# Kernel optimization log

Hardware: AMD Instinct MI355X
Metric: run time of the kernel (lower is better)

The kernel has to match this reference:

```python
import jax, jax.numpy as jnp
import numpy as np
import math


def setup_inputs() -> dict:
    key = jax.random.key(0)
    k0, k1, k2, k3, k4 = jax.random.split(key, 5)
    in_f, out_f, nb = 512, 512, 8
    B, S = 4, 2048
    x = jax.random.normal(k0, (B, S, in_f), dtype=jnp.float32)
    # RBF params (frozen in original: basis_trainable=False)
    fan_in = in_f  # fan_in of rbf.weight.T which is (num_basis, in_features)
    bound = 1.0 / math.sqrt(fan_in)
    rbf_weight = jax.random.uniform(k1, (in_f, nb), dtype=jnp.float32,
                                    minval=-math.sqrt(3.0) * 0.33 / math.sqrt(fan_in),
                                    maxval=math.sqrt(3.0) * 0.33 / math.sqrt(fan_in))
    rbf_centers = jnp.tile(jnp.linspace(-bound, bound, nb, dtype=jnp.float32)[None, :], (in_f, 1))
    # KAN spline weight (in, nb, out); fan_in for init is in_f*nb
    fan2 = in_f * nb
    wb = math.sqrt(3.0) * 0.33 / math.sqrt(fan2)
    weight = jax.random.uniform(k2, (in_f, nb, out_f), dtype=jnp.float32, minval=-wb, maxval=wb)
    bias = jax.random.uniform(k3, (out_f,), dtype=jnp.float32,
                              minval=-1.0 / math.sqrt(fan2), maxval=1.0 / math.sqrt(fan2))
    scale_base = jax.random.uniform(k4, (in_f, out_f), dtype=jnp.float32, minval=-0.1, maxval=0.1)
    return {"x": x, "rbf_weight": rbf_weight, "rbf_centers": rbf_centers,
            "weight": weight, "bias": bias, "scale_base": scale_base}


def reference(x, rbf_weight, rbf_centers, weight, bias, scale_base):
    in_f = x.shape[-1]
    nb = rbf_weight.shape[1]
    beta = (nb / math.log2(nb)) ** 2  # get_rbf_width(2/nb, log2(nb))
    batch_shape = x.shape[:-1]
    xf = x.reshape(-1, in_f)  # (N, in)
    # RBF basis expansion: (N, in, nb)
    z = xf[:, :, None] * rbf_weight[None, :, :] - rbf_centers[None, :, :]
    phi = jnp.exp(-beta * (z * z))
    # spline contraction + base path, expressed as efficient contractions
    y = jnp.einsum('nib,ibo->no', phi, weight)
    y = y + bias + jnp.cos(xf) @ scale_base
    return y.reshape(*batch_shape, weight.shape[-1])
```

## Files before the change

### kernel.cpp

```cpp
#include <hip/hip_runtime.h>
#include <hip/hip_bf16.h>

typedef __attribute__((ext_vector_type(8))) short short8;
typedef __attribute__((ext_vector_type(4))) float f32x4;

#define IN_F 512
#define OUT_F 512
#define BM 64
#define BN 512
#define BK 64
#define THREADS 512
#define PHI_STEPS 64
#define NSTEPS 72
#define KSPLIT 2
#define SPL (NSTEPS / KSPLIT)
#define IMG_CHUNKS 4096
#define A_SH (BM * BK)
#define B_SH (BN * BK)
#define PART_ELEMS (8192 * OUT_F)

__device__ __forceinline__ short f2bf(float f) {
  __hip_bfloat16 h = __float2bfloat16(f);
  return __builtin_bit_cast(short, h);
}

__device__ __forceinline__ void glds16(const void* g, void* l) {
  __builtin_amdgcn_global_load_lds(
      (const __attribute__((address_space(1))) unsigned int*)g,
      (__attribute__((address_space(3))) unsigned int*)l, 16, 0, 0);
}

__device__ __forceinline__ float bsrc(const float* __restrict__ w,
                                      const float* __restrict__ sb,
                                      int k, int col) {
  return (k < IN_F * 8) ? w[(size_t)k * OUT_F + col]
                        : sb[(size_t)(k - IN_F * 8) * OUT_F + col];
}

__global__ void __launch_bounds__(256) prep_b(const float* __restrict__ w,
                                              const float* __restrict__ sb,
                                              short* __restrict__ img) {
  const int D = blockIdx.x * 256 + threadIdx.x;
  const int ci = D & (IMG_CHUNKS - 1);
  const int s = D >> 12;
  const int n = ci >> 3, slot = ci & 7;
  const int oct = slot ^ (n & 7);
  short8 v;
#pragma unroll
  for (int j = 0; j < 8; ++j) v[j] = f2bf(bsrc(w, sb, s * 64 + oct * 8 + j, n));
  *(short8*)&img[(size_t)D * 8] = v;
}

__global__ void __launch_bounds__(256) reduce_add(const float* __restrict__ part,
                                                  float* __restrict__ out) {
  const int n4 = PART_ELEMS / 4;
  const float4* p4 = (const float4*)part;
  float4* o4 = (float4*)out;
  for (int i = blockIdx.x * 256 + threadIdx.x; i < n4; i += gridDim.x * 256) {
    float4 a = o4[i];
    const float4 b = p4[i];
    a.x += b.x; a.y += b.y; a.z += b.z; a.w += b.w;
    o4[i] = a;
  }
}

template <int KS, bool PREB>
__global__ void __launch_bounds__(THREADS, 2) kan_main(
    const float* __restrict__ x, const float* __restrict__ rw,
    const float* __restrict__ rc, const float* __restrict__ w,
    const float* __restrict__ bias, const float* __restrict__ sb,
    const short* __restrict__ bimg, float* __restrict__ out,
    float* __restrict__ part) {
  __shared__ __align__(16) short A_lds[2][A_SH];
  __shared__ __align__(16) short B_lds[2][B_SH];

  const int t = threadIdx.x, lane = t & 63, wid = t >> 6;
  const int l15 = lane & 15, kb = lane >> 4;
  const int m0 = blockIdx.x * BM;
  const int ks = (KS == 2) ? blockIdx.y : 0;
  const int s0 = ks * SPL;

  const int a_il = t & 7;
  const int a_m = t >> 3;
  const float c2 = -10.2591705f;

  f32x4 acc[4][4];
#pragma unroll
  for (int i = 0; i < 4; ++i)
#pragma unroll
    for (int j = 0; j < 4; ++j) acc[i][j] = (f32x4){0.f, 0.f, 0.f, 0.f};

  auto stage = [&](int s, short* __restrict__ Ad, short* __restrict__ Bd) {
    if (PREB) {
      const short* src = bimg + ((size_t)s * IMG_CHUNKS + t) * 8;
#pragma unroll
      for (int c = 0; c < 8; ++c)
        glds16(src + (size_t)c * 512 * 8, Bd + c * 4096 + wid * 512);
    } else {
#pragma unroll
      for (int c = 0; c < 8; ++c) {
        const int ci = c * 512 + t;
        const int n = ci >> 3, slot = ci & 7, oct = slot ^ (n & 7);
        short8 v;
#pragma unroll
        for (int j = 0; j < 8; ++j) v[j] = f2bf(bsrc(w, sb, s * 64 + oct * 8 + j, n));
        *(short8*)&Bd[ci * 8] = v;
      }
    }
    short8 av;
    if (s < PHI_STEPS) {
      const int feat = s * 8 + a_il;
      const float xv = x[(size_t)(m0 + a_m) * IN_F + feat];
      const float4 r0 = *(const float4*)(rw + feat * 8);
      const float4 r1 = *(const float4*)(rw + feat * 8 + 4);
      const float4 q0 = *(const float4*)(rc + feat * 8);
      const float4 q1 = *(const float4*)(rc + feat * 8 + 4);
      const float rwv[8] = {r0.x, r0.y, r0.z, r0.w, r1.x, r1.y, r1.z, r1.w};
      const float rcv[8] = {q0.x, q0.y, q0.z, q0.w, q1.x, q1.y, q1.z, q1.w};
#pragma unroll
      for (int b = 0; b < 8; ++b) {
        const float z = fmaf(xv, rwv[b], -rcv[b]);
        av[b] = f2bf(exp2f(c2 * z * z));
      }
    } else {
      const float* xp = x + (size_t)(m0 + a_m) * IN_F + (s - PHI_STEPS) * 64 + a_il * 8;
      const float4 xa = *(const float4*)xp;
      const float4 xb = *(const float4*)(xp + 4);
      av[0] = f2bf(__cosf(xa.x)); av[1] = f2bf(__cosf(xa.y));
      av[2] = f2bf(__cosf(xa.z)); av[3] = f2bf(__cosf(xa.w));
      av[4] = f2bf(__cosf(xb.x)); av[5] = f2bf(__cosf(xb.y));
      av[6] = f2bf(__cosf(xb.z)); av[7] = f2bf(__cosf(xb.w));
    }
    Ad[a_m * BK + (a_il ^ (a_m & 7)) * 8 + 0] = av[0];
    *(short8*)&Ad[a_m * BK + (a_il ^ (a_m & 7)) * 8] = av;
  };

  auto mfma_step = [&](const short* __restrict__ Ab, const short* __restrict__ Bb) {
#pragma unroll
    for (int kk = 0; kk < 2; ++kk) {
      const int sk = kk * 4 + kb;
      short8 af[4], bf[4];
#pragma unroll
      for (int mi = 0; mi < 4; ++mi) {
        const int r = mi * 16 + l15;
        af[mi] = *(const short8*)&Ab[r * BK + (sk ^ (r & 7)) * 8];
      }
#pragma unroll
      for (int ni = 0; ni < 4; ++ni) {
        const int n = wid * 64 + ni * 16 + l15;
        bf[ni] = *(const short8*)&Bb[n * BK + (sk ^ (n & 7)) * 8];
      }
#pragma unroll
      for (int mi = 0; mi < 4; ++mi)
#pragma unroll
        for (int ni = 0; ni < 4; ++ni)
          acc[mi][ni] = __builtin_amdgcn_mfma_f32_16x16x32_bf16(
              af[mi], bf[ni], acc[mi][ni], 0, 0, 0);
    }
  };

  stage(s0, A_lds[0], B_lds[0]);
  __syncthreads();
#pragma unroll 2
  for (int si = 0; si < SPL; ++si) {
    const int cur = si & 1;
    if (si + 1 < SPL) stage(s0 + si + 1, A_lds[cur ^ 1], B_lds[cur ^ 1]);
    mfma_step(A_lds[cur], B_lds[cur]);
    __syncthreads();
  }

#pragma unroll
  for (int ni = 0; ni < 4; ++ni) {
    const int col = wid * 64 + ni * 16 + l15;
    const float bb = (KS == 1 || ks == 0) ? bias[col] : 0.f;
#pragma unroll
    for (int mi = 0; mi < 4; ++mi) {
      const int rb = m0 + mi * 16 + kb * 4;
#pragma unroll
      for (int r4 = 0; r4 < 4; ++r4) {
        const size_t idx = (size_t)(rb + r4) * OUT_F + col;
        if (KS == 1 || ks == 0) out[idx] = acc[mi][ni][r4] + bb;
        else                    part[idx] = acc[mi][ni][r4];
      }
    }
  }
}

extern "C" void kernel_launch(void* const* d_in, const int* in_sizes, int n_in,
                              void* d_out, int out_size, void* d_ws, size_t ws_size,
                              hipStream_t stream) {
  const float* x    = (const float*)d_in[0];
  const float* rw   = (const float*)d_in[1];
  const float* rc   = (const float*)d_in[2];
  const float* w    = (const float*)d_in[3];
  const float* bias = (const float*)d_in[4];
  const float* sb   = (const float*)d_in[5];
  float* out = (float*)d_out;

  const int nrows = in_sizes[0] / IN_F;

  const size_t img_bytes  = (size_t)NSTEPS * IMG_CHUNKS * 16;
  const size_t part_bytes = (size_t)PART_ELEMS * sizeof(float);
  const int img_chunks_total = NSTEPS * IMG_CHUNKS;

  if (ws_size >= img_bytes + part_bytes) {
    short* img = (short*)d_ws;
    float* part = (float*)((char*)d_ws + img_bytes);
    prep_b<<<img_chunks_total / 256, 256, 0, stream>>>(w, sb, img);
    dim3 grid(nrows / BM, KSPLIT);
    kan_main<KSPLIT, true><<<grid, THREADS, 0, stream>>>(x, rw, rc, w, bias, sb,
                                                         img, out, part);
    reduce_add<<<2048, 256, 0, stream>>>(part, out);
  } else if (ws_size >= part_bytes) {
    float* part = (float*)d_ws;
    dim3 grid(nrows / BM, KSPLIT);
    kan_main<KSPLIT, false><<<grid, THREADS, 0, stream>>>(x, rw, rc, w, bias, sb,
                                                          nullptr, out, part);
    reduce_add<<<2048, 256, 0, stream>>>(part, out);
  } else {
    dim3 grid(nrows / BM, 1);
    kan_main<1, false><<<grid, THREADS, 0, stream>>>(x, rw, rc, w, bias, sb,
                                                     nullptr, out, nullptr);
  }
}
```

Measured before the change: 85.15 us.

## Rewrite KAN kernel with 256x256 tiles, 4-way K-split, bf16 partials

Replaces the 64-row, full-N tile kernel with 1024-thread blocks computing 256x256 output tiles over a 4-way K-split. A new pre-pass transposes x into a per-feature layout so it can be streamed into LDS with async global-to-LDS loads, and each wave computes phi for one feature octet across rows. Partial sums from three of the splits are stored as bf16 and combined by a three-way reduce kernel. Barriers and waitcnts are placed by hand. The aim is more reuse of A and B per tile and less partial-sum traffic. The costs are an extra transpose pass, a larger workspace, lost precision in the bf16 partials, and the removal of the workspace-size fallbacks.

```diff
diff --git a/kernel.cpp b/kernel.cpp
--- a/kernel.cpp
+++ b/kernel.cpp
@@ -6,28 +6,32 @@
 
 #define IN_F 512
 #define OUT_F 512
-#define BM 64
-#define BN 512
-#define BK 64
-#define THREADS 512
 #define PHI_STEPS 64
 #define NSTEPS 72
-#define KSPLIT 2
-#define SPL (NSTEPS / KSPLIT)
-#define IMG_CHUNKS 4096
-#define A_SH (BM * BK)
-#define B_SH (BN * BK)
+#define BCH2 2048
+#define NT2 2
+#define KT 18
 #define PART_ELEMS (8192 * OUT_F)
+#define C2 (-10.2591705f)
 
 __device__ __forceinline__ short f2bf(float f) {
-  __hip_bfloat16 h = __float2bfloat16(f);
-  return __builtin_bit_cast(short, h);
+  unsigned u = __builtin_bit_cast(unsigned, f);
+  u += 0x7fffu + ((u >> 16) & 1u);
+  return (short)(u >> 16);
+}
+__device__ __forceinline__ float b2f(unsigned short u) {
+  return __builtin_bit_cast(float, (unsigned)u << 16);
 }
 
 __device__ __forceinline__ void glds16(const void* g, void* l) {
   __builtin_amdgcn_global_load_lds(
       (const __attribute__((address_space(1))) unsigned int*)g,
       (__attribute__((address_space(3))) unsigned int*)l, 16, 0, 0);
+}
+__device__ __forceinline__ void glds4(const void* g, void* l) {
+  __builtin_amdgcn_global_load_lds(
+      (const __attribute__((address_space(1))) unsigned int*)g,
+      (__attribute__((address_space(3))) unsigned int*)l, 4, 0, 0);
 }
 
 __device__ __forceinline__ float bsrc(const float* __restrict__ w,
@@ -37,52 +41,86 @@
                         : sb[(size_t)(k - IN_F * 8) * OUT_F + col];
 }
 
-__global__ void __launch_bounds__(256) prep_b(const float* __restrict__ w,
-                                              const float* __restrict__ sb,
-                                              short* __restrict__ img) {
+__global__ void __launch_bounds__(256) prep_b2(const float* __restrict__ w,
+                                               const float* __restrict__ sb,
+                                               short* __restrict__ img) {
   const int D = blockIdx.x * 256 + threadIdx.x;
-  const int ci = D & (IMG_CHUNKS - 1);
-  const int s = D >> 12;
+  const int ci = D & (BCH2 - 1);
+  const int im = D >> 11;
+  const int s = im % NSTEPS;
+  const int nt = im / NSTEPS;
   const int n = ci >> 3, slot = ci & 7;
   const int oct = slot ^ (n & 7);
+  const int col = nt * 256 + n;
   short8 v;
 #pragma unroll
-  for (int j = 0; j < 8; ++j) v[j] = f2bf(bsrc(w, sb, s * 64 + oct * 8 + j, n));
+  for (int j = 0; j < 8; ++j) v[j] = f2bf(bsrc(w, sb, s * 64 + oct * 8 + j, col));
   *(short8*)&img[(size_t)D * 8] = v;
 }
 
-__global__ void __launch_bounds__(256) reduce_add(const float* __restrict__ part,
-                                                  float* __restrict__ out) {
+__global__ void __launch_bounds__(256) prep_x(const float* __restrict__ x,
+                                              float* __restrict__ ximg) {
+  __shared__ float T[256][17];
+  const int t = threadIdx.x;
+  const int s2 = blockIdx.x;
+  const int blk = blockIdx.y;
+#pragma unroll
+  for (int rep = 0; rep < 4; ++rep) {
+    const int row = rep * 64 + (t >> 2);
+    const int p = t & 3;
+    const float4 v = *(const float4*)&x[(size_t)(blk * 256 + row) * IN_F + s2 * 16 + p * 4];
+    T[row][p * 4 + 0] = v.x; T[row][p * 4 + 1] = v.y;
+    T[row][p * 4 + 2] = v.z; T[row][p * 4 + 3] = v.w;
+  }
+  __syncthreads();
+#pragma unroll
+  for (int f = 0; f < 16; ++f) {
+    const int s = 2 * s2 + (f >> 3), oct = f & 7;
+    ximg[(size_t)s * 65536 + oct * 8192 + blk * 256 + t] = T[t][f];
+  }
+}
+
+__global__ void __launch_bounds__(256) reduce3b(const short* __restrict__ part,
+                                                float* __restrict__ out) {
+  typedef __attribute__((ext_vector_type(4))) short short4v;
   const int n4 = PART_ELEMS / 4;
-  const float4* p4 = (const float4*)part;
+  const short4v* p0 = (const short4v*)part;
+  const short4v* p1 = (const short4v*)(part + PART_ELEMS);
+  const short4v* p2 = (const short4v*)(part + 2 * (size_t)PART_ELEMS);
   float4* o4 = (float4*)out;
   for (int i = blockIdx.x * 256 + threadIdx.x; i < n4; i += gridDim.x * 256) {
     float4 a = o4[i];
-    const float4 b = p4[i];
-    a.x += b.x; a.y += b.y; a.z += b.z; a.w += b.w;
+    const short4v q0 = p0[i], q1 = p1[i], q2 = p2[i];
+    a.x += b2f((unsigned short)q0[0]) + b2f((unsigned short)q1[0]) + b2f((unsigned short)q2[0]);
+    a.y += b2f((unsigned short)q0[1]) + b2f((unsigned short)q1[1]) + b2f((unsigned short)q2[1]);
+    a.z += b2f((unsigned short)q0[2]) + b2f((unsigned short)q1[2]) + b2f((unsigned short)q2[2]);
+    a.w += b2f((unsigned short)q0[3]) + b2f((unsigned short)q1[3]) + b2f((unsigned short)q2[3]);
     o4[i] = a;
   }
 }
 
-template <int KS, bool PREB>
-__global__ void __launch_bounds__(THREADS, 2) kan_main(
-    const float* __restrict__ x, const float* __restrict__ rw,
-    const float* __restrict__ rc, const float* __restrict__ w,
-    const float* __restrict__ bias, const float* __restrict__ sb,
-    const short* __restrict__ bimg, float* __restrict__ out,
-    float* __restrict__ part) {
-  __shared__ __align__(16) short A_lds[2][A_SH];
-  __shared__ __align__(16) short B_lds[2][B_SH];
+__device__ __forceinline__ f32x4 MFMA(short8 a, short8 b, f32x4 c) {
+  return __builtin_amdgcn_mfma_f32_16x16x32_bf16(a, b, c, 0, 0, 0);
+}
+
+__global__ void __launch_bounds__(1024, 4) kan_fx(
+    const float* __restrict__ x, const float* __restrict__ ximg,
+    const float* __restrict__ rw, const float* __restrict__ rc,
+    const short* __restrict__ bimg, const float* __restrict__ bias,
+    float* __restrict__ out, short* __restrict__ part) {
+  __shared__ __align__(16) short A_lds[2][256 * 64];
+  __shared__ __align__(16) short B_lds[2][256 * 64];
+  __shared__ __align__(16) float X_lds[2][2048];
 
   const int t = threadIdx.x, lane = t & 63, wid = t >> 6;
+  const int wm = wid >> 2, wn = wid & 3;
   const int l15 = lane & 15, kb = lane >> 4;
-  const int m0 = blockIdx.x * BM;
-  const int ks = (KS == 2) ? blockIdx.y : 0;
-  const int s0 = ks * SPL;
-
-  const int a_il = t & 7;
-  const int a_m = t >> 3;
-  const float c2 = -10.2591705f;
+  const int mb = blockIdx.x, nt = blockIdx.y, ks = blockIdx.z;
+  const int m0 = mb * 256, n0 = nt * 256, s0 = ks * KT;
+
+  const int octu = __builtin_amdgcn_readfirstlane(wid >> 1);
+  const int h = wid & 1;
+  const int r1 = h * 128 + lane, r2 = r1 + 64;
 
   f32x4 acc[4][4];
 #pragma unroll
@@ -90,97 +128,130 @@
 #pragma unroll
     for (int j = 0; j < 4; ++j) acc[i][j] = (f32x4){0.f, 0.f, 0.f, 0.f};
 
-  auto stage = [&](int s, short* __restrict__ Ad, short* __restrict__ Bd) {
-    if (PREB) {
-      const short* src = bimg + ((size_t)s * IMG_CHUNKS + t) * 8;
-#pragma unroll
-      for (int c = 0; c < 8; ++c)
-        glds16(src + (size_t)c * 512 * 8, Bd + c * 4096 + wid * 512);
-    } else {
-#pragma unroll
-      for (int c = 0; c < 8; ++c) {
-        const int ci = c * 512 + t;
-        const int n = ci >> 3, slot = ci & 7, oct = slot ^ (n & 7);
-        short8 v;
-#pragma unroll
-        for (int j = 0; j < 8; ++j) v[j] = f2bf(bsrc(w, sb, s * 64 + oct * 8 + j, n));
-        *(short8*)&Bd[ci * 8] = v;
-      }
-    }
-    short8 av;
-    if (s < PHI_STEPS) {
-      const int feat = s * 8 + a_il;
-      const float xv = x[(size_t)(m0 + a_m) * IN_F + feat];
-      const float4 r0 = *(const float4*)(rw + feat * 8);
-      const float4 r1 = *(const float4*)(rw + feat * 8 + 4);
-      const float4 q0 = *(const float4*)(rc + feat * 8);
-      const float4 q1 = *(const float4*)(rc + feat * 8 + 4);
-      const float rwv[8] = {r0.x, r0.y, r0.z, r0.w, r1.x, r1.y, r1.z, r1.w};
-      const float rcv[8] = {q0.x, q0.y, q0.z, q0.w, q1.x, q1.y, q1.z, q1.w};
-#pragma unroll
-      for (int b = 0; b < 8; ++b) {
-        const float z = fmaf(xv, rwv[b], -rcv[b]);
-        av[b] = f2bf(exp2f(c2 * z * z));
-      }
-    } else {
-      const float* xp = x + (size_t)(m0 + a_m) * IN_F + (s - PHI_STEPS) * 64 + a_il * 8;
-      const float4 xa = *(const float4*)xp;
-      const float4 xb = *(const float4*)(xp + 4);
-      av[0] = f2bf(__cosf(xa.x)); av[1] = f2bf(__cosf(xa.y));
-      av[2] = f2bf(__cosf(xa.z)); av[3] = f2bf(__cosf(xa.w));
-      av[4] = f2bf(__cosf(xb.x)); av[5] = f2bf(__cosf(xb.y));
-      av[6] = f2bf(__cosf(xb.z)); av[7] = f2bf(__cosf(xb.w));
-    }
-    Ad[a_m * BK + (a_il ^ (a_m & 7)) * 8 + 0] = av[0];
-    *(short8*)&Ad[a_m * BK + (a_il ^ (a_m & 7)) * 8] = av;
-  };
-
-  auto mfma_step = [&](const short* __restrict__ Ab, const short* __restrict__ Bb) {
+  float rwv[8], rcv[8];
+
+  auto loadP = [&](int s1) {
+    const int feat = s1 * 8 + octu;
+#pragma unroll
+    for (int j = 0; j < 8; ++j) { rwv[j] = rw[feat * 8 + j]; rcv[j] = rc[feat * 8 + j]; }
+  };
+  auto stageX = [&](int s1, int buf) {
+    const float* base = ximg + (size_t)s1 * 65536 + octu * 8192 + mb * 256 + h * 128;
+    glds4(base + lane, &X_lds[buf][wid * 128]);
+    glds4(base + 64 + lane, &X_lds[buf][wid * 128 + 64]);
+  };
+  auto stageB = [&](int s1, int buf) {
+#pragma unroll
+    for (int c = 0; c < 2; ++c) {
+      const short* src = bimg + (((size_t)nt * NSTEPS + s1) * BCH2 + c * 1024 + t) * 8;
+      glds16(src, &B_lds[buf][c * 8192 + wid * 512]);
+    }
+  };
+  auto writeA_phi = [&](int buf) {
+    const float xa = X_lds[buf][wid * 128 + lane];
+    const float xb = X_lds[buf][wid * 128 + 64 + lane];
+    short8 va, vb;
+#pragma unroll
+    for (int b = 0; b < 8; ++b) {
+      const float za = fmaf(xa, rwv[b], -rcv[b]);
+      const float zb = fmaf(xb, rwv[b], -rcv[b]);
+      va[b] = f2bf(exp2f(C2 * za * za));
+      vb[b] = f2bf(exp2f(C2 * zb * zb));
+    }
+    *(short8*)&A_lds[buf][r1 * 64 + (octu ^ (r1 & 7)) * 8] = va;
+    *(short8*)&A_lds[buf][r2 * 64 + (octu ^ (r2 & 7)) * 8] = vb;
+  };
+  auto writeA_cos = [&](int buf, const float4& a0, const float4& a1,
+                        const float4& b0, const float4& b1) {
+    short8 va, vb;
+    va[0] = f2bf(__cosf(a0.x)); va[1] = f2bf(__cosf(a0.y));
+    va[2] = f2bf(__cosf(a0.z)); va[3] = f2bf(__cosf(a0.w));
+    va[4] = f2bf(__cosf(a1.x)); va[5] = f2bf(__cosf(a1.y));
+    va[6] = f2bf(__cosf(a1.z)); va[7] = f2bf(__cosf(a1.w));
+    vb[0] = f2bf(__cosf(b0.x)); vb[1] = f2bf(__cosf(b0.y));
+    vb[2] = f2bf(__cosf(b0.z)); vb[3] = f2bf(__cosf(b0.w));
+    vb[4] = f2bf(__cosf(b1.x)); vb[5] = f2bf(__cosf(b1.y));
+    vb[6] = f2bf(__cosf(b1.z)); vb[7] = f2bf(__cosf(b1.w));
+    *(short8*)&A_lds[buf][r1 * 64 + (octu ^ (r1 & 7)) * 8] = va;
+    *(short8*)&A_lds[buf][r2 * 64 + (octu ^ (r2 & 7)) * 8] = vb;
+  };
+  auto mma = [&](int buf) {
 #pragma unroll
     for (int kk = 0; kk < 2; ++kk) {
       const int sk = kk * 4 + kb;
       short8 af[4], bf[4];
 #pragma unroll
       for (int mi = 0; mi < 4; ++mi) {
-        const int r = mi * 16 + l15;
-        af[mi] = *(const short8*)&Ab[r * BK + (sk ^ (r & 7)) * 8];
+        const int r = wm * 64 + mi * 16 + l15;
+        af[mi] = *(const short8*)&A_lds[buf][r * 64 + (sk ^ (r & 7)) * 8];
       }
 #pragma unroll
       for (int ni = 0; ni < 4; ++ni) {
-        const int n = wid * 64 + ni * 16 + l15;
-        bf[ni] = *(const short8*)&Bb[n * BK + (sk ^ (n & 7)) * 8];
+        const int n = wn * 64 + ni * 16 + l15;
+        bf[ni] = *(const short8*)&B_lds[buf][n * 64 + (sk ^ (n & 7)) * 8];
       }
 #pragma unroll
       for (int mi = 0; mi < 4; ++mi)
 #pragma unroll
         for (int ni = 0; ni < 4; ++ni)
-          acc[mi][ni] = __builtin_amdgcn_mfma_f32_16x16x32_bf16(
-              af[mi], bf[ni], acc[mi][ni], 0, 0, 0);
-    }
-  };
-
-  stage(s0, A_lds[0], B_lds[0]);
-  __syncthreads();
-#pragma unroll 2
-  for (int si = 0; si < SPL; ++si) {
-    const int cur = si & 1;
-    if (si + 1 < SPL) stage(s0 + si + 1, A_lds[cur ^ 1], B_lds[cur ^ 1]);
-    mfma_step(A_lds[cur], B_lds[cur]);
-    __syncthreads();
+          acc[mi][ni] = MFMA(af[mi], bf[ni], acc[mi][ni]);
+    }
+  };
+
+  loadP(s0);
+  stageX(s0, 0);
+  stageB(s0, 0);
+  asm volatile("s_waitcnt vmcnt(2)" ::: "memory");
+  writeA_phi(0);
+  asm volatile("s_waitcnt lgkmcnt(0)" ::: "memory");
+
+  for (int si = 0; si < KT; ++si) {
+    const int b = si & 1;
+    const int s = s0 + si;
+    const bool hasN = (si + 1 < KT);
+    const bool nPhi = (s + 1 < PHI_STEPS);
+    float4 ca0, ca1, cb0, cb1;
+    if (hasN) {
+      if (nPhi) {
+        loadP(s + 1);
+        stageX(s + 1, b ^ 1);
+        stageB(s + 1, b ^ 1);
+        asm volatile("s_waitcnt vmcnt(4)" ::: "memory");
+      } else {
+        const int f0 = (s + 1 - PHI_STEPS) * 64 + octu * 8;
+        const float* xr1 = x + (size_t)(m0 + r1) * IN_F + f0;
+        const float* xr2 = x + (size_t)(m0 + r2) * IN_F + f0;
+        ca0 = *(const float4*)xr1; ca1 = *(const float4*)(xr1 + 4);
+        cb0 = *(const float4*)xr2; cb1 = *(const float4*)(xr2 + 4);
+        stageB(s + 1, b ^ 1);
+        asm volatile("s_waitcnt vmcnt(2)" ::: "memory");
+      }
+    } else {
+      asm volatile("s_waitcnt vmcnt(0)" ::: "memory");
+    }
+    __builtin_amdgcn_s_barrier();
+    mma(b);
+    if (hasN) {
+      asm volatile("s_waitcnt vmcnt(2)" ::: "memory");
+      if (nPhi) writeA_phi(b ^ 1);
+      else      writeA_cos(b ^ 1, ca0, ca1, cb0, cb1);
+      asm volatile("s_waitcnt lgkmcnt(0)" ::: "memory");
+    }
+    __builtin_amdgcn_s_barrier();
   }
 
 #pragma unroll
   for (int ni = 0; ni < 4; ++ni) {
-    const int col = wid * 64 + ni * 16 + l15;
-    const float bb = (KS == 1 || ks == 0) ? bias[col] : 0.f;
+    const int col = n0 + wn * 64 + ni * 16 + l15;
+    const float bb = (ks == 0) ? bias[col] : 0.f;
 #pragma unroll
     for (int mi = 0; mi < 4; ++mi) {
-      const int rb = m0 + mi * 16 + kb * 4;
+      const int rb = m0 + wm * 64 + mi * 16 + kb * 4;
 #pragma unroll
       for (int r4 = 0; r4 < 4; ++r4) {
         const size_t idx = (size_t)(rb + r4) * OUT_F + col;
-        if (KS == 1 || ks == 0) out[idx] = acc[mi][ni][r4] + bb;
-        else                    part[idx] = acc[mi][ni][r4];
+        if (ks == 0) out[idx] = acc[mi][ni][r4] + bb;
+        else         part[(size_t)(ks - 1) * PART_ELEMS + idx] = f2bf(acc[mi][ni][r4]);
       }
     }
   }
@@ -199,27 +270,18 @@
 
   const int nrows = in_sizes[0] / IN_F;
 
-  const size_t img_bytes  = (size_t)NSTEPS * IMG_CHUNKS * 16;
-  const size_t part_bytes = (size_t)PART_ELEMS * sizeof(float);
-  const int img_chunks_total = NSTEPS * IMG_CHUNKS;
-
-  if (ws_size >= img_bytes + part_bytes) {
-    short* img = (short*)d_ws;
-    float* part = (float*)((char*)d_ws + img_bytes);
-    prep_b<<<img_chunks_total / 256, 256, 0, stream>>>(w, sb, img);
-    dim3 grid(nrows / BM, KSPLIT);
-    kan_main<KSPLIT, true><<<grid, THREADS, 0, stream>>>(x, rw, rc, w, bias, sb,
-                                                         img, out, part);
-    reduce_add<<<2048, 256, 0, stream>>>(part, out);
-  } else if (ws_size >= part_bytes) {
-    float* part = (float*)d_ws;
-    dim3 grid(nrows / BM, KSPLIT);
-    kan_main<KSPLIT, false><<<grid, THREADS, 0, stream>>>(x, rw, rc, w, bias, sb,
-                                                          nullptr, out, part);
-    reduce_add<<<2048, 256, 0, stream>>>(part, out);
-  } else {
-    dim3 grid(nrows / BM, 1);
-    kan_main<1, false><<<grid, THREADS, 0, stream>>>(x, rw, rc, w, bias, sb,
-                                                     nullptr, out, nullptr);
-  }
-}
+  const size_t b_bytes    = (size_t)NT2 * NSTEPS * BCH2 * 16;
+  const size_t x_bytes    = (size_t)PHI_STEPS * 65536 * 4;
+  const size_t p_bytes    = (size_t)3 * PART_ELEMS * sizeof(short);
+
+  short* bimg = (short*)d_ws;
+  float* ximg = (float*)((char*)d_ws + b_bytes);
+  short* part = (short*)((char*)d_ws + b_bytes + x_bytes);
+  (void)ws_size;
+
+  prep_b2<<<NT2 * NSTEPS * BCH2 / 256, 256, 0, stream>>>(w, sb, bimg);
+  prep_x<<<dim3(32, 32), 256, 0, stream>>>(x, ximg);
+  kan_fx<<<dim3(nrows / 256, 2, 4), 1024, 0, stream>>>(x, ximg, rw, rc,
+                                                       bimg, bias, out, part);
+  reduce3b<<<2048, 256, 0, stream>>>(part, out);
+}
```

Result: slower. 100.3 us (+17.8%).
